# Optimization experiments

Hardware: AMD Instinct MI355X
Metric: run time of the kernel (lower is better)

Reference implementation:

```python
import jax, jax.numpy as jnp
import numpy as np

N, E, IN_C, HID, HEADS, OUT_C, NG = 50000, 800000, 300, 64, 2, 2, 256


def _lin(key, fan_in, fan_out):
    k1, k2 = jax.random.split(key)
    lim = 1.0 / np.sqrt(fan_in)
    W = jax.random.uniform(k1, (fan_in, fan_out), jnp.float32, -lim, lim)
    b = jax.random.uniform(k2, (fan_out,), jnp.float32, -lim, lim)
    return W, b


def setup_inputs() -> dict:
    key = jax.random.key(0)
    ks = jax.random.split(key, 16)
    x = jax.random.normal(ks[0], (N, IN_C), jnp.float32)
    edge_index = jax.random.randint(ks[1], (2, E), 0, N, jnp.int64)
    batch = jnp.sort(jax.random.randint(ks[2], (N,), 0, NG, jnp.int64))
    d = {"x": x, "edge_index": edge_index, "batch": batch}
    d["syn_W"], d["syn_b"] = _lin(ks[3], IN_C, HID)
    d["ant_W"], d["ant_b"] = _lin(ks[4], IN_C, HID)
    d["fus_W"], d["fus_b"] = _lin(ks[5], 2 * HID, HID * HEADS)
    # conv1: in=HID*HEADS, out=HID, heads=HEADS (concat)
    d["c1_Wq"], d["c1_bq"] = _lin(ks[6], HID * HEADS, HEADS * HID)
    d["c1_Wk"], d["c1_bk"] = _lin(ks[7], HID * HEADS, HEADS * HID)
    d["c1_Wv"], d["c1_bv"] = _lin(ks[8], HID * HEADS, HEADS * HID)
    d["c1_Ws"], d["c1_bs"] = _lin(ks[9], HID * HEADS, HEADS * HID)
    # conv2: in=HID*HEADS, out=HID, heads=1
    d["c2_Wq"], d["c2_bq"] = _lin(ks[10], HID * HEADS, HID)
    d["c2_Wk"], d["c2_bk"] = _lin(ks[11], HID * HEADS, HID)
    d["c2_Wv"], d["c2_bv"] = _lin(ks[12], HID * HEADS, HID)
    d["c2_Ws"], d["c2_bs"] = _lin(ks[13], HID * HEADS, HID)
    d["l1_W"], d["l1_b"] = _lin(ks[14], HID, HID)
    d["l2_W"], d["l2_b"] = _lin(ks[15], HID, OUT_C)
    return d


def transformer_conv(x, src, dst, Wq, bq, Wk, bk, Wv, bv, Ws, bs, heads, d_head):
    # PyG TransformerConv (concat=True, root_weight=True, eval mode)
    q = (x @ Wq + bq).reshape(-1, heads, d_head)  # [N,H,D]
    k = (x @ Wk + bk).reshape(-1, heads, d_head)
    v = (x @ Wv + bv).reshape(-1, heads, d_head)
    qi = q[dst]  # [E,H,D]
    kj = k[src]
    vj = v[src]
    alpha = jnp.einsum("ehd,ehd->eh", qi, kj) / jnp.sqrt(jnp.float32(d_head))
    amax = jax.ops.segment_max(alpha, dst, num_segments=x.shape[0])
    ealpha = jnp.exp(alpha - amax[dst])
    denom = jax.ops.segment_sum(ealpha, dst, num_segments=x.shape[0])
    alpha = ealpha / (denom[dst] + 1e-16)
    out = jax.ops.segment_sum(alpha[..., None] * vj, dst, num_segments=x.shape[0])
    out = out.reshape(x.shape[0], heads * d_head)
    return out + x @ Ws + bs


def reference(x, edge_index, batch, syn_W, syn_b, ant_W, ant_b, fus_W, fus_b,
              c1_Wq, c1_bq, c1_Wk, c1_bk, c1_Wv, c1_bv, c1_Ws, c1_bs,
              c2_Wq, c2_bq, c2_Wk, c2_bk, c2_Wv, c2_bv, c2_Ws, c2_bs,
              l1_W, l1_b, l2_W, l2_b):
    src, dst = edge_index[0], edge_index[1]
    x_syn = jax.nn.relu(x @ syn_W + syn_b)
    x_ant = jax.nn.relu(x @ ant_W + ant_b)
    x_fused = jnp.concatenate([x_syn, x_ant], axis=1) @ fus_W + fus_b  # [N, HID*HEADS]
    h = transformer_conv(x_fused, src, dst, c1_Wq, c1_bq, c1_Wk, c1_bk,
                         c1_Wv, c1_bv, c1_Ws, c1_bs, HEADS, HID)
    h = jax.nn.relu(h)
    h = transformer_conv(h, src, dst, c2_Wq, c2_bq, c2_Wk, c2_bk,
                         c2_Wv, c2_bv, c2_Ws, c2_bs, 1, HID)
    # global mean pool over graphs
    sums = jax.ops.segment_sum(h, batch, num_segments=NG)
    cnts = jax.ops.segment_sum(jnp.ones((h.shape[0], 1), h.dtype), batch, num_segments=NG)
    pooled = sums / jnp.maximum(cnts, 1.0)
    out = jax.nn.relu(pooled @ l1_W + l1_b)
    return out @ l2_W + l2_b
```

## Files before the change

kernel.cpp:

```cpp
#include <hip/hip_runtime.h>
#include <math.h>

#define NNODES 50000
#define NEDGES 800000
#define INC    300
#define NGRAPH 256

typedef __attribute__((ext_vector_type(8))) short bf16x8;
typedef __attribute__((ext_vector_type(4))) short bf16x4;
typedef __attribute__((ext_vector_type(4))) float f32x4;

#define L2E8 0.180336880f
#define SW(row, k) ((k) ^ (((row) & 7) << 3))
#define EB 3125
#define FRONT_BLOCKS 782
#define FF_GRID (FRONT_BLOCKS + EB)

__device__ __forceinline__ unsigned short f2bf(float f) {
    unsigned u = __float_as_uint(f);
    u += 0x7fffu + ((u >> 16) & 1u);
    return (unsigned short)(u >> 16);
}
__device__ __forceinline__ float bf2f(unsigned short h) {
    return __uint_as_float(((unsigned)h) << 16);
}

struct WTArgs {
    const float* w[11];
    unsigned short* o[11];
    int K[11];
    int N[11];
    int mode[11];
    int roff[11];
    const float* syn_b; const float* ant_b;
    const float* c1q; const float* c1k; const float* c1v; const float* c1s;
    const float* c2q; const float* c2k; const float* c2v; const float* c2s;
    float* enc_b;
    float* c1_b;
    float* c2_b;
};

__global__ void k_setup(WTArgs a, const int* __restrict__ dstv, int* __restrict__ deg) {
    int bx = blockIdx.x;
    if (bx < EB) {
        int e = bx * 256 + threadIdx.x;
        if (e < NEDGES) atomicAdd(&deg[dstv[e]], 1);
        return;
    }
    bx -= EB;
    int which = bx / 75;
    int sub = bx - which * 75;
    if (which == 11) {
        if (sub != 0) return;
        int t = threadIdx.x;
        for (int u = t; u < 896; u += 256) {
            if (u < 512) {
                int s = u >> 7, r = u & 127;
                const float* p = (s == 0) ? a.c1q : (s == 1) ? a.c1k : (s == 2) ? a.c1v : a.c1s;
                a.c1_b[u] = p[r];
            } else if (u < 768) {
                int v = u - 512;
                int s = v >> 6, r = v & 63;
                const float* p = (s == 0) ? a.c2q : (s == 1) ? a.c2k : (s == 2) ? a.c2v : a.c2s;
                a.c2_b[v] = p[r];
            } else {
                int v = u - 768;
                a.enc_b[v] = (v < 64) ? a.syn_b[v] : a.ant_b[v - 64];
            }
        }
        return;
    }
    int i = sub * 256 + threadIdx.x;
    int K = a.K[which], N = a.N[which];
    if (i >= K * N) return;
    int k = i / N, n = i - k * N;
    unsigned short v = f2bf(a.w[which][i]);
    size_t dst;
    int m = a.mode[which];
    if (m == 1) {
        int row = a.roff[which] + n;
        dst = (size_t)(k >> 6) * 8192 + row * 64 + SW(row, k & 63);
    } else if (m == 2) {
        dst = (size_t)n * 128 + SW(n, k);
    } else {
        dst = (size_t)n * K + k;
    }
    a.o[which][dst] = v;
}

__global__ void k_scan1(const int* __restrict__ deg, int* __restrict__ ex,
                        int* __restrict__ bsum, int n) {
    __shared__ int tmp[256];
    int i = blockIdx.x * 256 + threadIdx.x;
    int v = (i < n) ? deg[i] : 0;
    tmp[threadIdx.x] = v;
    __syncthreads();
    for (int off = 1; off < 256; off <<= 1) {
        int t = (threadIdx.x >= off) ? tmp[threadIdx.x - off] : 0;
        __syncthreads();
        tmp[threadIdx.x] += t;
        __syncthreads();
    }
    if (i < n) ex[i] = tmp[threadIdx.x] - v;
    if (threadIdx.x == 255) bsum[blockIdx.x] = tmp[255];
}

__global__ void k_scan3(int* __restrict__ rp, const int* __restrict__ bsum,
                        int* __restrict__ cursor, int n, int E, int nb) {
    __shared__ int tmp[256];
    int t = threadIdx.x;
    int v = (t < nb && t < (int)blockIdx.x) ? bsum[t] : 0;
    tmp[t] = v;
    __syncthreads();
    for (int off = 128; off > 0; off >>= 1) {
        if (t < off) tmp[t] += tmp[t + off];
        __syncthreads();
    }
    int boff = tmp[0];
    int i = blockIdx.x * 256 + t;
    if (i < n) {
        int r = rp[i] + boff;
        rp[i] = r;
        cursor[i] = r;
    }
    if (i == 0) rp[n] = E;
}

__global__ __launch_bounds__(256) void k_front_fill(
    const float* __restrict__ x,
    const unsigned short* __restrict__ enc_img, const float* __restrict__ enc_b,
    const unsigned short* __restrict__ fus_img, const float* __restrict__ fus_b,
    const unsigned short* __restrict__ c1_img, const float* __restrict__ c1_b,
    unsigned short* __restrict__ qkvs1, int M,
    const int* __restrict__ src, const int* __restrict__ dstv,
    int* __restrict__ cursor, int* __restrict__ esrc)
{
    const int b = blockIdx.x;
    const int q = b / 5, r5 = b - q * 5;
    const int tid = threadIdx.x;
    if (!(r5 == 0 && q < FRONT_BLOCKS)) {
        int nf = (b + 4) / 5;
        if (nf > FRONT_BLOCKS) nf = FRONT_BLOCKS;
        int e = (b - nf) * 256 + tid;
        if (e < NEDGES) {
            int d = dstv[e];
            int p = atomicAdd(&cursor[d], 1);
            esrc[p] = src[e];
        }
        return;
    }
    __shared__ __align__(16) short P[16384];
    short* bufI = P;
    short* Bh   = P + 8192;
    const int bm = q * 64;
    const int l  = tid & 63;
    const int wv = tid >> 6;
    const int fr = l & 15;
    const int fg = l >> 4;

    bf16x8 aP[10];
    {
        int row = bm + wv * 16 + fr;
        if (row >= M) row = M - 1;
        const float* xr = x + (size_t)row * INC + fg * 8;
        #pragma unroll
        for (int t = 0; t < 9; ++t) {
            float4 u0 = *reinterpret_cast<const float4*>(xr + t * 32);
            float4 u1 = *reinterpret_cast<const float4*>(xr + t * 32 + 4);
            bf16x8 f;
            f[0] = (short)f2bf(u0.x); f[1] = (short)f2bf(u0.y);
            f[2] = (short)f2bf(u0.z); f[3] = (short)f2bf(u0.w);
            f[4] = (short)f2bf(u1.x); f[5] = (short)f2bf(u1.y);
            f[6] = (short)f2bf(u1.z); f[7] = (short)f2bf(u1.w);
            aP[t] = f;
        }
        bf16x8 f9 = (bf16x8){0, 0, 0, 0, 0, 0, 0, 0};
        int c0 = 288 + fg * 8;
        #pragma unroll
        for (int j = 0; j < 8; ++j) {
            int c = c0 + j;
            if (c < INC) f9[j] = (short)f2bf(x[(size_t)row * INC + c]);
        }
        aP[9] = f9;
    }

    f32x4 acc1[8];
    #pragma unroll
    for (int j = 0; j < 8; ++j) acc1[j] = (f32x4){0.f, 0.f, 0.f, 0.f};

    for (int ph = 0; ph < 5; ++ph) {
        {
            bf16x8* d = (bf16x8*)Bh;
            const bf16x8* s = (const bf16x8*)(enc_img + ph * 8192);
            #pragma unroll
            for (int i = 0; i < 4; ++i) d[tid + i * 256] = s[tid + i * 256];
        }
        __syncthreads();
        #pragma unroll
        for (int ks = 0; ks < 2; ++ks) {
            int kk = ks * 32 + fg * 8;
            int t = ph * 2 + ks;
            #pragma unroll
            for (int nj = 0; nj < 8; ++nj) {
                int br = nj * 16 + fr;
                bf16x8 bfr = *reinterpret_cast<const bf16x8*>(Bh + br * 64 + SW(br, kk));
                acc1[nj] = __builtin_amdgcn_mfma_f32_16x16x32_bf16(aP[t], bfr, acc1[nj], 0, 0, 0);
            }
        }
        __syncthreads();
    }
    #pragma unroll
    for (int nj = 0; nj < 8; ++nj) {
        int col = nj * 16 + fr;
        float bv = enc_b[col];
        #pragma unroll
        for (int r = 0; r < 4; ++r) {
            int row = wv * 16 + fg * 4 + r;
            float val = fmaxf(acc1[nj][r] + bv, 0.f);
            bufI[row * 128 + SW(row, col)] = (short)f2bf(val);
        }
    }
    __syncthreads();

    bf16x8 af[4];
    {
        int ar = wv * 16 + fr;
        #pragma unroll
        for (int t = 0; t < 4; ++t)
            af[t] = *reinterpret_cast<const bf16x8*>(bufI + ar * 128 + SW(ar, fg * 8 + t * 32));
    }

    f32x4 acc2[8];
    #pragma unroll
    for (int j = 0; j < 8; ++j) acc2[j] = (f32x4){0.f, 0.f, 0.f, 0.f};
    #pragma unroll
    for (int h = 0; h < 2; ++h) {
        __syncthreads();
        {
            bf16x8* d = (bf16x8*)Bh;
            const bf16x8* s = (const bf16x8*)(fus_img + h * 64 * 128);
            #pragma unroll
            for (int i = 0; i < 4; ++i) d[tid + i * 256] = s[tid + i * 256];
        }
        __syncthreads();
        #pragma unroll
        for (int t = 0; t < 4; ++t) {
            int k = t * 32 + fg * 8;
            #pragma unroll
            for (int nj = 0; nj < 4; ++nj) {
                int br = nj * 16 + fr;
                bf16x8 bfr = *reinterpret_cast<const bf16x8*>(Bh + br * 128 + SW(br, k));
                acc2[h * 4 + nj] = __builtin_amdgcn_mfma_f32_16x16x32_bf16(af[t], bfr, acc2[h * 4 + nj], 0, 0, 0);
            }
        }
    }
    __syncthreads();
    #pragma unroll
    for (int h = 0; h < 2; ++h)
        #pragma unroll
        for (int nj = 0; nj < 4; ++nj) {
            int col = h * 64 + nj * 16 + fr;
            float bv = fus_b[col];
            #pragma unroll
            for (int r = 0; r < 4; ++r) {
                int row = wv * 16 + fg * 4 + r;
                bufI[row * 128 + SW(row, col)] = (short)f2bf(acc2[h * 4 + nj][r] + bv);
            }
        }
    __syncthreads();

    bf16x8 af2[4];
    {
        int ar = wv * 16 + fr;
        #pragma unroll
        for (int t = 0; t < 4; ++t)
            af2[t] = *reinterpret_cast<const bf16x8*>(bufI + ar * 128 + SW(ar, fg * 8 + t * 32));
    }

    #pragma unroll
    for (int cc = 0; cc < 4; ++cc) {
        f32x4 acc3[8];
        #pragma unroll
        for (int j = 0; j < 8; ++j) acc3[j] = (f32x4){0.f, 0.f, 0.f, 0.f};
        #pragma unroll
        for (int h = 0; h < 2; ++h) {
            __syncthreads();
            {
                bf16x8* d = (bf16x8*)Bh;
                const bf16x8* s = (const bf16x8*)(c1_img + cc * 16384 + h * 64 * 128);
                #pragma unroll
                for (int i = 0; i < 4; ++i) d[tid + i * 256] = s[tid + i * 256];
            }
            __syncthreads();
            #pragma unroll
            for (int t = 0; t < 4; ++t) {
                int k = t * 32 + fg * 8;
                #pragma unroll
                for (int nj = 0; nj < 4; ++nj) {
                    int br = nj * 16 + fr;
                    bf16x8 bfr = *reinterpret_cast<const bf16x8*>(Bh + br * 128 + SW(br, k));
                    acc3[h * 4 + nj] = __builtin_amdgcn_mfma_f32_16x16x32_bf16(af2[t], bfr, acc3[h * 4 + nj], 0, 0, 0);
                }
            }
        }
        #pragma unroll
        for (int h = 0; h < 2; ++h)
            #pragma unroll
            for (int nj = 0; nj < 4; ++nj) {
                int col = h * 64 + nj * 16 + fr;
                float bv = c1_b[cc * 128 + col];
                #pragma unroll
                for (int r = 0; r < 4; ++r) {
                    int row = wv * 16 + fg * 4 + r;
                    bufI[row * 128 + col] = (short)f2bf(acc3[h * 4 + nj][r] + bv);
                }
            }
        __syncthreads();
        #pragma unroll
        for (int i = 0; i < 4; ++i) {
            int p = tid + i * 256;
            int row = p >> 4;
            int c8 = (p & 15) * 8;
            int gr = bm + row;
            if (gr < M)
                *reinterpret_cast<bf16x8*>(qkvs1 + (size_t)gr * 512 + cc * 128 + c8) =
                    *reinterpret_cast<const bf16x8*>(bufI + row * 128 + c8);
        }
    }
}

#define BM 128

template<int BNT>
__global__ __launch_bounds__(256) void gemm_mfma(
    const unsigned short* __restrict__ A, int lda, int M, int K,
    const unsigned short* __restrict__ Wt,
    const float* __restrict__ bias,
    unsigned short* __restrict__ C, int ldc)
{
    __shared__ __align__(16) short As[BM * 64];
    __shared__ __align__(16) short Bs[BNT * 64];
    const int tid = threadIdx.x;
    const int bm = blockIdx.x * BM;
    const int bn = blockIdx.y * BNT;
    const int tr = tid >> 4;
    const int tc = (tid & 15) * 4;
    const int l  = tid & 63;
    const int wv = tid >> 6;
    const int fr = l & 15;
    const int fg = l >> 4;

    f32x4 acc[2][BNT / 16];
    #pragma unroll
    for (int i = 0; i < 2; ++i)
        #pragma unroll
        for (int j = 0; j < BNT / 16; ++j) acc[i][j] = (f32x4){0.f, 0.f, 0.f, 0.f};

    for (int k0 = 0; k0 < K; k0 += 64) {
        #pragma unroll
        for (int p = 0; p < 8; ++p) {
            int row = p * 16 + tr;
            int grow = bm + row;
            int k = k0 + tc;
            bf16x4 s4 = (bf16x4){0, 0, 0, 0};
            if (grow < M) s4 = *reinterpret_cast<const bf16x4*>(A + (size_t)grow * lda + k);
            *reinterpret_cast<bf16x4*>(As + row * 64 + SW(row, tc)) = s4;
        }
        #pragma unroll
        for (int p = 0; p < BNT / 16; ++p) {
            int n = p * 16 + tr;
            *reinterpret_cast<bf16x4*>(Bs + n * 64 + SW(n, tc)) =
                *reinterpret_cast<const bf16x4*>(Wt + (size_t)(bn + n) * K + k0 + tc);
        }
        __syncthreads();
        #pragma unroll
        for (int ks = 0; ks < 2; ++ks) {
            int kk = ks * 32 + fg * 8;
            int ar0 = wv * 32 + fr, ar1 = wv * 32 + 16 + fr;
            bf16x8 a0 = *reinterpret_cast<const bf16x8*>(As + ar0 * 64 + SW(ar0, kk));
            bf16x8 a1 = *reinterpret_cast<const bf16x8*>(As + ar1 * 64 + SW(ar1, kk));
            #pragma unroll
            for (int nj = 0; nj < BNT / 16; ++nj) {
                int br = nj * 16 + fr;
                bf16x8 b = *reinterpret_cast<const bf16x8*>(Bs + br * 64 + SW(br, kk));
                acc[0][nj] = __builtin_amdgcn_mfma_f32_16x16x32_bf16(a0, b, acc[0][nj], 0, 0, 0);
                acc[1][nj] = __builtin_amdgcn_mfma_f32_16x16x32_bf16(a1, b, acc[1][nj], 0, 0, 0);
            }
        }
        __syncthreads();
    }
    #pragma unroll
    for (int mi = 0; mi < 2; ++mi) {
        #pragma unroll
        for (int nj = 0; nj < BNT / 16; ++nj) {
            int col = nj * 16 + fr;
            float bv = bias[bn + col];
            #pragma unroll
            for (int r = 0; r < 4; ++r) {
                int lr = wv * 16 + fg * 4 + r;
                As[lr * BNT + col] = (short)f2bf(acc[mi][nj][r] + bv);
            }
        }
        __syncthreads();
        #pragma unroll
        for (int i = 0; i < 4; ++i) {
            int p = tid + i * 256;
            int lr = p >> 4;
            int c8 = (p & 15) * 8;
            int grow = bm + (lr >> 4) * 32 + mi * 16 + (lr & 15);
            if (grow < M)
                *reinterpret_cast<bf16x8*>(C + (size_t)grow * ldc + bn + c8) =
                    *reinterpret_cast<const bf16x8*>(As + lr * BNT + c8);
        }
        __syncthreads();
    }
}

__global__ __launch_bounds__(256) void attn_h2(
    const unsigned short* __restrict__ qkvs,
    const int* __restrict__ rowptr, const int* __restrict__ esrc,
    unsigned short* __restrict__ outp, int N)
{
    int wid = (blockIdx.x * blockDim.x + threadIdx.x) >> 6;
    int l = threadIdx.x & 63;
    if (wid >= N) return;
    const int sl = l & 15;
    const int g  = l >> 4;
    const unsigned short* bi = qkvs + (size_t)wid * 512;
    float q[8];
    {
        bf16x8 qv = *reinterpret_cast<const bf16x8*>(bi + 8 * sl);
        #pragma unroll
        for (int i = 0; i < 8; ++i) q[i] = bf2f((unsigned short)qv[i]) * L2E8;
    }
    float s = 0.f;
    float acc[8] = {0.f, 0.f, 0.f, 0.f, 0.f, 0.f, 0.f, 0.f};
    const int beg = rowptr[wid], end = rowptr[wid + 1];
    const int iters = (end - beg + 3) >> 2;
    int e = beg + g;
    bool va0 = e < end;
    int j0 = va0 ? esrc[e] : wid;
    const unsigned short* pp0 = qkvs + (size_t)j0 * 512 + 8 * sl;
    bf16x8 ka = *reinterpret_cast<const bf16x8*>(pp0 + 128);
    bf16x8 vva = *reinterpret_cast<const bf16x8*>(pp0 + 256);
    bool va1 = (e + 4) < end;
    int j1 = va1 ? esrc[e + 4] : wid;
    const unsigned short* pp1 = qkvs + (size_t)j1 * 512 + 8 * sl;
    bf16x8 kb = *reinterpret_cast<const bf16x8*>(pp1 + 128);
    bf16x8 vvb = *reinterpret_cast<const bf16x8*>(pp1 + 256);
    for (int it = 0; it < iters; ++it) {
        bf16x8 kc = ka, vc = vva;
        bool vd = va0;
        ka = kb; vva = vvb; va0 = va1;
        va1 = (e + 8) < end;
        int j2 = va1 ? esrc[e + 8] : wid;
        const unsigned short* p2 = qkvs + (size_t)j2 * 512 + 8 * sl;
        kb = *reinterpret_cast<const bf16x8*>(p2 + 128);
        vvb = *reinterpret_cast<const bf16x8*>(p2 + 256);
        e += 4;
        float p = 0.f;
        #pragma unroll
        for (int i = 0; i < 8; ++i) p += q[i] * bf2f((unsigned short)kc[i]);
        p += __shfl_xor(p, 1, 64);
        p += __shfl_xor(p, 2, 64);
        p += __shfl_xor(p, 4, 64);
        float w = vd ? __builtin_amdgcn_exp2f(p) : 0.f;
        s += w;
        #pragma unroll
        for (int i = 0; i < 8; ++i) acc[i] += w * bf2f((unsigned short)vc[i]);
    }
    #pragma unroll
    for (int mask = 16; mask <= 32; mask <<= 1) {
        s += __shfl_xor(s, mask, 64);
        #pragma unroll
        for (int i = 0; i < 8; ++i) acc[i] += __shfl_xor(acc[i], mask, 64);
    }
    if (g == 0) {
        float inv = 1.f / (s + 1e-16f);
        bf16x8 sv = *reinterpret_cast<const bf16x8*>(bi + 384 + 8 * sl);
        bf16x8 o;
        #pragma unroll
        for (int i = 0; i < 8; ++i) {
            float r = fmaxf(acc[i] * inv + bf2f((unsigned short)sv[i]), 0.f);
            o[i] = (short)f2bf(r);
        }
        *reinterpret_cast<bf16x8*>(outp + (size_t)wid * 128 + 8 * sl) = o;
    }
}

__global__ __launch_bounds__(256) void attn_h1(
    const unsigned short* __restrict__ qkvs,
    const int* __restrict__ rowptr, const int* __restrict__ esrc,
    float* __restrict__ outp, int N)
{
    int wid = (blockIdx.x * blockDim.x + threadIdx.x) >> 6;
    int l = threadIdx.x & 63;
    if (wid >= N) return;
    const int sl = l & 7;
    const int g  = l >> 3;
    const unsigned short* bi = qkvs + (size_t)wid * 256;
    float q[8];
    {
        bf16x8 qv = *reinterpret_cast<const bf16x8*>(bi + 8 * sl);
        #pragma unroll
        for (int i = 0; i < 8; ++i) q[i] = bf2f((unsigned short)qv[i]) * L2E8;
    }
    float s = 0.f;
    float acc[8] = {0.f, 0.f, 0.f, 0.f, 0.f, 0.f, 0.f, 0.f};
    const int beg = rowptr[wid], end = rowptr[wid + 1];
    const int iters = (end - beg + 7) >> 3;
    int e = beg + g;
    bool va0 = e < end;
    int j0 = va0 ? esrc[e] : wid;
    const unsigned short* pp0 = qkvs + (size_t)j0 * 256 + 8 * sl;
    bf16x8 ka = *reinterpret_cast<const bf16x8*>(pp0 + 64);
    bf16x8 vva = *reinterpret_cast<const bf16x8*>(pp0 + 128);
    bool va1 = (e + 8) < end;
    int j1 = va1 ? esrc[e + 8] : wid;
    const unsigned short* pp1 = qkvs + (size_t)j1 * 256 + 8 * sl;
    bf16x8 kb = *reinterpret_cast<const bf16x8*>(pp1 + 64);
    bf16x8 vvb = *reinterpret_cast<const bf16x8*>(pp1 + 128);
    for (int it = 0; it < iters; ++it) {
        bf16x8 kc = ka, vc = vva;
        bool vd = va0;
        ka = kb; vva = vvb; va0 = va1;
        va1 = (e + 16) < end;
        int j2 = va1 ? esrc[e + 16] : wid;
        const unsigned short* p2 = qkvs + (size_t)j2 * 256 + 8 * sl;
        kb = *reinterpret_cast<const bf16x8*>(p2 + 64);
        vvb = *reinterpret_cast<const bf16x8*>(p2 + 128);
        e += 8;
        float p = 0.f;
        #pragma unroll
        for (int i = 0; i < 8; ++i) p += q[i] * bf2f((unsigned short)kc[i]);
        p += __shfl_xor(p, 1, 64);
        p += __shfl_xor(p, 2, 64);
        p += __shfl_xor(p, 4, 64);
        float w = vd ? __builtin_amdgcn_exp2f(p) : 0.f;
        s += w;
        #pragma unroll
        for (int i = 0; i < 8; ++i) acc[i] += w * bf2f((unsigned short)vc[i]);
    }
    #pragma unroll
    for (int mask = 8; mask <= 32; mask <<= 1) {
        s += __shfl_xor(s, mask, 64);
        #pragma unroll
        for (int i = 0; i < 8; ++i) acc[i] += __shfl_xor(acc[i], mask, 64);
    }
    if (g == 0) {
        float inv = 1.f / (s + 1e-16f);
        float r[8];
        #pragma unroll
        for (int i = 0; i < 8; ++i)
            r[i] = acc[i] * inv + bf2f(bi[192 + 8 * sl + i]);
        float* op = outp + (size_t)wid * 64 + 8 * sl;
        *reinterpret_cast<float4*>(op)     = make_float4(r[0], r[1], r[2], r[3]);
        *reinterpret_cast<float4*>(op + 4) = make_float4(r[4], r[5], r[6], r[7]);
    }
}

__device__ __forceinline__ int lbound(const int* __restrict__ a, int n, int key) {
    int lo = 0, hi = n;
    while (lo < hi) {
        int mid = (lo + hi) >> 1;
        if (a[mid] < key) lo = mid + 1; else hi = mid;
    }
    return lo;
}

__global__ void pool_head(const float* __restrict__ h, const int* __restrict__ batch,
                          const float* __restrict__ l1W, const float* __restrict__ l1b,
                          const float* __restrict__ l2W, const float* __restrict__ l2b,
                          float* __restrict__ out) {
    __shared__ float red[4][64];
    int g = blockIdx.x;
    int l = threadIdx.x & 63;
    int w = threadIdx.x >> 6;
    int lo = lbound(batch, NNODES, g);
    int hi = lbound(batch, NNODES, g + 1);
    float s = 0.f;
    for (int i = lo + w; i < hi; i += 4) s += h[(size_t)i * 64 + l];
    red[w][l] = s;
    __syncthreads();
    if (w == 0) {
        float t = red[0][l] + red[1][l] + red[2][l] + red[3][l];
        float cnt = (float)((hi - lo) > 1 ? (hi - lo) : 1);
        float p = t / cnt;
        float hsum = l1b[l];
        #pragma unroll
        for (int kk = 0; kk < 64; ++kk) {
            float pk = __shfl(p, kk, 64);
            hsum += pk * l1W[kk * 64 + l];
        }
        float hr = fmaxf(hsum, 0.f);
        float o0 = hr * l2W[l * 2 + 0];
        float o1 = hr * l2W[l * 2 + 1];
        #pragma unroll
        for (int off = 32; off > 0; off >>= 1) {
            o0 += __shfl_xor(o0, off, 64);
            o1 += __shfl_xor(o1, off, 64);
        }
        if (l == 0) {
            out[g * 2 + 0] = o0 + l2b[0];
            out[g * 2 + 1] = o1 + l2b[1];
        }
    }
}

extern "C" void kernel_launch(void* const* d_in, const int* in_sizes, int n_in,
                              void* d_out, int out_size, void* d_ws, size_t ws_size,
                              hipStream_t stream) {
    const float* x      = (const float*)d_in[0];
    const int*   ei     = (const int*)d_in[1];
    const int*   batch  = (const int*)d_in[2];
    const float* syn_W  = (const float*)d_in[3];  const float* syn_b = (const float*)d_in[4];
    const float* ant_W  = (const float*)d_in[5];  const float* ant_b = (const float*)d_in[6];
    const float* fus_W  = (const float*)d_in[7];  const float* fus_b = (const float*)d_in[8];
    const float* c1_Wq  = (const float*)d_in[9];  const float* c1_bq = (const float*)d_in[10];
    const float* c1_Wk  = (const float*)d_in[11]; const float* c1_bk = (const float*)d_in[12];
    const float* c1_Wv  = (const float*)d_in[13]; const float* c1_bv = (const float*)d_in[14];
    const float* c1_Ws  = (const float*)d_in[15]; const float* c1_bs = (const float*)d_in[16];
    const float* c2_Wq  = (const float*)d_in[17]; const float* c2_bq = (const float*)d_in[18];
    const float* c2_Wk  = (const float*)d_in[19]; const float* c2_bk = (const float*)d_in[20];
    const float* c2_Wv  = (const float*)d_in[21]; const float* c2_bv = (const float*)d_in[22];
    const float* c2_Ws  = (const float*)d_in[23]; const float* c2_bs = (const float*)d_in[24];
    const float* l1_W   = (const float*)d_in[25]; const float* l1_b  = (const float*)d_in[26];
    const float* l2_W   = (const float*)d_in[27]; const float* l2_b  = (const float*)d_in[28];
    const int* src = ei;
    const int* dst = ei + NEDGES;
    float* out = (float*)d_out;

    char* ws = (char*)d_ws;
    size_t off = 0;
    auto alloc = [&](size_t bytes) -> char* {
        char* p = ws + off;
        off += (bytes + 255) & ~((size_t)255);
        return p;
    };

    unsigned short* H     = (unsigned short*)alloc((size_t)NNODES * 128 * 2);
    unsigned short* H2b   = (unsigned short*)alloc((size_t)NNODES * 128 * 2);
    unsigned short* qkvs1 = (unsigned short*)alloc((size_t)NNODES * 512 * 2);
    unsigned short* qkvs2 = (unsigned short*)alloc((size_t)NNODES * 256 * 2);
    unsigned short* fus_img = (unsigned short*)alloc((size_t)16384 * 2);
    unsigned short* c1_img  = (unsigned short*)alloc((size_t)4 * 16384 * 2);
    unsigned short* c2w_t   = (unsigned short*)alloc((size_t)256 * 128 * 2);
    float* enc_b = (float*)alloc(128 * 4);
    float* c1_b  = (float*)alloc(512 * 4);
    float* c2_b  = (float*)alloc(256 * 4);
    int*   cursor = (int*)alloc((NNODES + 1) * 4);
    int*   rowptr = (int*)alloc((NNODES + 1) * 4);
    int*   bsum   = (int*)alloc(256 * 4);
    int*   esrc   = (int*)alloc((size_t)NEDGES * 4);
    char* zbase = ws + off;
    int*   deg     = (int*)alloc((NNODES + 1) * 4);
    unsigned short* enc_img = (unsigned short*)alloc((size_t)5 * 8192 * 2);
    size_t zspan = (size_t)((ws + off) - zbase);

    const int NB = (NNODES + 255) / 256;
    dim3 t256(256);

    WTArgs wa;
    wa.w[0] = syn_W;  wa.o[0] = enc_img;  wa.K[0] = 300; wa.N[0] = 64;  wa.mode[0] = 1; wa.roff[0] = 0;
    wa.w[1] = ant_W;  wa.o[1] = enc_img;  wa.K[1] = 300; wa.N[1] = 64;  wa.mode[1] = 1; wa.roff[1] = 64;
    wa.w[2] = fus_W;  wa.o[2] = fus_img;  wa.K[2] = 128; wa.N[2] = 128; wa.mode[2] = 2; wa.roff[2] = 0;
    wa.w[3] = c1_Wq;  wa.o[3] = c1_img + 0 * 16384; wa.K[3] = 128; wa.N[3] = 128; wa.mode[3] = 2; wa.roff[3] = 0;
    wa.w[4] = c1_Wk;  wa.o[4] = c1_img + 1 * 16384; wa.K[4] = 128; wa.N[4] = 128; wa.mode[4] = 2; wa.roff[4] = 0;
    wa.w[5] = c1_Wv;  wa.o[5] = c1_img + 2 * 16384; wa.K[5] = 128; wa.N[5] = 128; wa.mode[5] = 2; wa.roff[5] = 0;
    wa.w[6] = c1_Ws;  wa.o[6] = c1_img + 3 * 16384; wa.K[6] = 128; wa.N[6] = 128; wa.mode[6] = 2; wa.roff[6] = 0;
    wa.w[7] = c2_Wq;  wa.o[7] = c2w_t + 0 * 64 * 128;  wa.K[7] = 128; wa.N[7] = 64; wa.mode[7] = 0; wa.roff[7] = 0;
    wa.w[8] = c2_Wk;  wa.o[8] = c2w_t + 1 * 64 * 128;  wa.K[8] = 128; wa.N[8] = 64; wa.mode[8] = 0; wa.roff[8] = 0;
    wa.w[9] = c2_Wv;  wa.o[9] = c2w_t + 2 * 64 * 128;  wa.K[9] = 128; wa.N[9] = 64; wa.mode[9] = 0; wa.roff[9] = 0;
    wa.w[10] = c2_Ws; wa.o[10] = c2w_t + 3 * 64 * 128; wa.K[10] = 128; wa.N[10] = 64; wa.mode[10] = 0; wa.roff[10] = 0;
    wa.syn_b = syn_b; wa.ant_b = ant_b;
    wa.c1q = c1_bq; wa.c1k = c1_bk; wa.c1v = c1_bv; wa.c1s = c1_bs;
    wa.c2q = c2_bq; wa.c2k = c2_bk; wa.c2v = c2_bv; wa.c2s = c2_bs;
    wa.enc_b = enc_b; wa.c1_b = c1_b; wa.c2_b = c2_b;

    hipMemsetAsync(zbase, 0, zspan, stream);
    k_setup<<<EB + 900, t256, 0, stream>>>(wa, dst, deg);

    k_scan1<<<NB, t256, 0, stream>>>(deg, rowptr, bsum, NNODES);
    k_scan3<<<NB, t256, 0, stream>>>(rowptr, bsum, cursor, NNODES, NEDGES, NB);

    k_front_fill<<<FF_GRID, t256, 0, stream>>>(
        x, enc_img, enc_b, fus_img, fus_b, c1_img, c1_b, qkvs1, NNODES,
        src, dst, cursor, esrc);

    attn_h2<<<(NNODES * 64 + 255) / 256, t256, 0, stream>>>(qkvs1, rowptr, esrc, H, NNODES);

    gemm_mfma<128><<<dim3((NNODES + BM - 1) / BM, 2), t256, 0, stream>>>(
        H, 128, NNODES, 128, c2w_t, c2_b, qkvs2, 256);

    float* H2 = (float*)H2b;
    attn_h1<<<(NNODES * 64 + 255) / 256, t256, 0, stream>>>(qkvs2, rowptr, esrc, H2, NNODES);

    pool_head<<<NGRAPH, t256, 0, stream>>>(H2, batch, l1_W, l1_b, l2_W, l2_b, out);
}
```

Measured before the change: 243.5 us.

## Prefetch next weight tile into registers while MFMAs run on current tile

```diff
diff --git a/kernel.cpp b/kernel.cpp
--- a/kernel.cpp
+++ b/kernel.cpp
@@ -184,18 +184,22 @@
         aP[9] = f9;
     }
 
+    bf16x8 tmp0, tmp1, tmp2, tmp3;
+    #define LDT(srcp) { const bf16x8* s_ = (const bf16x8*)(srcp); \
+        tmp0 = s_[tid]; tmp1 = s_[tid + 256]; tmp2 = s_[tid + 512]; tmp3 = s_[tid + 768]; }
+    #define WRT() { bf16x8* d_ = (bf16x8*)Bh; \
+        d_[tid] = tmp0; d_[tid + 256] = tmp1; d_[tid + 512] = tmp2; d_[tid + 768] = tmp3; }
+
+    LDT(enc_img);
+    WRT();
+    __syncthreads();
+
     f32x4 acc1[8];
     #pragma unroll
     for (int j = 0; j < 8; ++j) acc1[j] = (f32x4){0.f, 0.f, 0.f, 0.f};
 
     for (int ph = 0; ph < 5; ++ph) {
-        {
-            bf16x8* d = (bf16x8*)Bh;
-            const bf16x8* s = (const bf16x8*)(enc_img + ph * 8192);
-            #pragma unroll
-            for (int i = 0; i < 4; ++i) d[tid + i * 256] = s[tid + i * 256];
-        }
-        __syncthreads();
+        LDT(ph < 4 ? enc_img + (ph + 1) * 8192 : fus_img);
         #pragma unroll
         for (int ks = 0; ks < 2; ++ks) {
             int kk = ks * 32 + fg * 8;
@@ -208,6 +212,8 @@
             }
         }
         __syncthreads();
+        WRT();
+        __syncthreads();
     }
     #pragma unroll
     for (int nj = 0; nj < 8; ++nj) {
@@ -233,28 +239,34 @@
     f32x4 acc2[8];
     #pragma unroll
     for (int j = 0; j < 8; ++j) acc2[j] = (f32x4){0.f, 0.f, 0.f, 0.f};
-    #pragma unroll
-    for (int h = 0; h < 2; ++h) {
-        __syncthreads();
-        {
-            bf16x8* d = (bf16x8*)Bh;
-            const bf16x8* s = (const bf16x8*)(fus_img + h * 64 * 128);
-            #pragma unroll
-            for (int i = 0; i < 4; ++i) d[tid + i * 256] = s[tid + i * 256];
-        }
-        __syncthreads();
-        #pragma unroll
-        for (int t = 0; t < 4; ++t) {
-            int k = t * 32 + fg * 8;
-            #pragma unroll
-            for (int nj = 0; nj < 4; ++nj) {
-                int br = nj * 16 + fr;
-                bf16x8 bfr = *reinterpret_cast<const bf16x8*>(Bh + br * 128 + SW(br, k));
-                acc2[h * 4 + nj] = __builtin_amdgcn_mfma_f32_16x16x32_bf16(af[t], bfr, acc2[h * 4 + nj], 0, 0, 0);
-            }
-        }
-    }
-    __syncthreads();
+
+    LDT(fus_img + 64 * 128);
+    #pragma unroll
+    for (int t = 0; t < 4; ++t) {
+        int k = t * 32 + fg * 8;
+        #pragma unroll
+        for (int nj = 0; nj < 4; ++nj) {
+            int br = nj * 16 + fr;
+            bf16x8 bfr = *reinterpret_cast<const bf16x8*>(Bh + br * 128 + SW(br, k));
+            acc2[nj] = __builtin_amdgcn_mfma_f32_16x16x32_bf16(af[t], bfr, acc2[nj], 0, 0, 0);
+        }
+    }
+    __syncthreads();
+    WRT();
+    __syncthreads();
+    LDT(c1_img);
+    #pragma unroll
+    for (int t = 0; t < 4; ++t) {
+        int k = t * 32 + fg * 8;
+        #pragma unroll
+        for (int nj = 0; nj < 4; ++nj) {
+            int br = nj * 16 + fr;
+            bf16x8 bfr = *reinterpret_cast<const bf16x8*>(Bh + br * 128 + SW(br, k));
+            acc2[4 + nj] = __builtin_amdgcn_mfma_f32_16x16x32_bf16(af[t], bfr, acc2[4 + nj], 0, 0, 0);
+        }
+    }
+    __syncthreads();
+    WRT();
     #pragma unroll
     for (int h = 0; h < 2; ++h)
         #pragma unroll
@@ -277,56 +289,59 @@
             af2[t] = *reinterpret_cast<const bf16x8*>(bufI + ar * 128 + SW(ar, fg * 8 + t * 32));
     }
 
-    #pragma unroll
-    for (int cc = 0; cc < 4; ++cc) {
-        f32x4 acc3[8];
-        #pragma unroll
-        for (int j = 0; j < 8; ++j) acc3[j] = (f32x4){0.f, 0.f, 0.f, 0.f};
-        #pragma unroll
-        for (int h = 0; h < 2; ++h) {
+    f32x4 acc3[8];
+    #pragma unroll
+    for (int s = 0; s < 8; ++s) {
+        int cc = s >> 1, h = s & 1;
+        if (h == 0) {
+            #pragma unroll
+            for (int j = 0; j < 8; ++j) acc3[j] = (f32x4){0.f, 0.f, 0.f, 0.f};
+        }
+        if (s < 7) LDT(c1_img + (s + 1) * 8192);
+        #pragma unroll
+        for (int t = 0; t < 4; ++t) {
+            int k = t * 32 + fg * 8;
+            #pragma unroll
+            for (int nj = 0; nj < 4; ++nj) {
+                int br = nj * 16 + fr;
+                bf16x8 bfr = *reinterpret_cast<const bf16x8*>(Bh + br * 128 + SW(br, k));
+                acc3[h * 4 + nj] = __builtin_amdgcn_mfma_f32_16x16x32_bf16(af2[t], bfr, acc3[h * 4 + nj], 0, 0, 0);
+            }
+        }
+        if (h == 0) {
             __syncthreads();
-            {
-                bf16x8* d = (bf16x8*)Bh;
-                const bf16x8* s = (const bf16x8*)(c1_img + cc * 16384 + h * 64 * 128);
+            WRT();
+            __syncthreads();
+        } else {
+            __syncthreads();
+            if (s < 7) WRT();
+            #pragma unroll
+            for (int hh = 0; hh < 2; ++hh)
                 #pragma unroll
-                for (int i = 0; i < 4; ++i) d[tid + i * 256] = s[tid + i * 256];
-            }
+                for (int nj = 0; nj < 4; ++nj) {
+                    int col = hh * 64 + nj * 16 + fr;
+                    float bv = c1_b[cc * 128 + col];
+                    #pragma unroll
+                    for (int r = 0; r < 4; ++r) {
+                        int row = wv * 16 + fg * 4 + r;
+                        bufI[row * 128 + col] = (short)f2bf(acc3[hh * 4 + nj][r] + bv);
+                    }
+                }
             __syncthreads();
             #pragma unroll
-            for (int t = 0; t < 4; ++t) {
-                int k = t * 32 + fg * 8;
-                #pragma unroll
-                for (int nj = 0; nj < 4; ++nj) {
-                    int br = nj * 16 + fr;
-                    bf16x8 bfr = *reinterpret_cast<const bf16x8*>(Bh + br * 128 + SW(br, k));
-                    acc3[h * 4 + nj] = __builtin_amdgcn_mfma_f32_16x16x32_bf16(af2[t], bfr, acc3[h * 4 + nj], 0, 0, 0);
-                }
+            for (int i = 0; i < 4; ++i) {
+                int p = tid + i * 256;
+                int row = p >> 4;
+                int c8 = (p & 15) * 8;
+                int gr = bm + row;
+                if (gr < M)
+                    *reinterpret_cast<bf16x8*>(qkvs1 + (size_t)gr * 512 + cc * 128 + c8) =
+                        *reinterpret_cast<const bf16x8*>(bufI + row * 128 + c8);
             }
         }
-        #pragma unroll
-        for (int h = 0; h < 2; ++h)
-            #pragma unroll
-            for (int nj = 0; nj < 4; ++nj) {
-                int col = h * 64 + nj * 16 + fr;
-                float bv = c1_b[cc * 128 + col];
-                #pragma unroll
-                for (int r = 0; r < 4; ++r) {
-                    int row = wv * 16 + fg * 4 + r;
-                    bufI[row * 128 + col] = (short)f2bf(acc3[h * 4 + nj][r] + bv);
-                }
-            }
-        __syncthreads();
-        #pragma unroll
-        for (int i = 0; i < 4; ++i) {
-            int p = tid + i * 256;
-            int row = p >> 4;
-            int c8 = (p & 15) * 8;
-            int gr = bm + row;
-            if (gr < M)
-                *reinterpret_cast<bf16x8*>(qkvs1 + (size_t)gr * 512 + cc * 128 + c8) =
-                    *reinterpret_cast<const bf16x8*>(bufI + row * 128 + c8);
-        }
-    }
+    }
+    #undef LDT
+    #undef WRT
 }
 
 #define BM 128
```

Result: no change. 240.6 us (median of 2 runs) (-1.2%).
